# Kernel optimization log

Hardware: AMD Instinct MI355X
Metric: run time of the kernel (lower is better)

The kernel has to match this reference:

```python
import jax, jax.numpy as jnp
import numpy as np

N_QUBITS = 4
N_LAYERS = 3
SHORT_W = 2048
LONG_W = 8192
BATCH = 2048


def _conv1d(x, w, b, pad):
    # x: [B, Cin, L], w: [Cout, Cin, K]
    y = jax.lax.conv_general_dilated(x, w, window_strides=(1,), padding=[(pad, pad)],
                                     dimension_numbers=("NCH", "OIH", "NCH"))
    return y + b[None, :, None]


def _ry_mat(t):
    c, s = jnp.cos(t / 2), jnp.sin(t / 2)
    return jnp.stack([jnp.stack([c, -s]), jnp.stack([s, c])]).astype(jnp.complex64)


def _rz_mat(a):
    return jnp.diag(jnp.stack([jnp.exp(-0.5j * a), jnp.exp(0.5j * a)])).astype(jnp.complex64)


def _rot_mat(phi, theta, omega):
    # PennyLane Rot(phi, theta, omega) = RZ(omega) @ RY(theta) @ RZ(phi)
    return _rz_mat(omega) @ _ry_mat(theta) @ _rz_mat(phi)


def _apply_1q(state, U, wire):
    state = jnp.tensordot(U, state, axes=((1,), (wire,)))
    return jnp.moveaxis(state, 0, wire)


def _apply_cnot(state, c, t):
    s0 = jax.lax.index_in_dim(state, 0, axis=c, keepdims=True)
    s1 = jax.lax.index_in_dim(state, 1, axis=c, keepdims=True)
    s1 = jnp.flip(s1, axis=t)
    return jnp.concatenate([s0, s1], axis=c)


def _circuit(x, w):
    # x: [4] real features, w: [3, 4, 3] StronglyEntanglingLayers weights
    state = jnp.zeros((2,) * N_QUBITS, jnp.complex64).at[(0,) * N_QUBITS].set(1.0)
    for i in range(N_QUBITS):
        state = _apply_1q(state, _ry_mat(jnp.pi * x[i]), i)
    for l in range(N_LAYERS):
        r = (l % (N_QUBITS - 1)) + 1  # default PennyLane ranges: 1,2,3
        for i in range(N_QUBITS):
            state = _apply_1q(state, _rot_mat(w[l, i, 0], w[l, i, 1], w[l, i, 2]), i)
        for i in range(N_QUBITS):
            state = _apply_cnot(state, i, (i + r) % N_QUBITS)
    probs = jnp.abs(state) ** 2
    zs = []
    for i in range(N_QUBITS):
        p = probs.sum(axis=tuple(a for a in range(N_QUBITS) if a != i))
        zs.append(p[0] - p[1])  # <PauliZ_i>
    return jnp.stack(zs)


def setup_inputs() -> dict:
    key = jax.random.key(0)
    ks = jax.random.split(key, 13)
    d = {}
    d["xs"] = jax.random.normal(ks[0], (BATCH, 1, SHORT_W), jnp.float32)
    d["xl"] = jax.random.normal(ks[1], (BATCH, 1, LONG_W), jnp.float32)
    d["cs_conv_w"] = jax.random.normal(ks[2], (8, 1, 3), jnp.float32) * 0.3
    d["cs_conv_b"] = jax.random.normal(ks[3], (8,), jnp.float32) * 0.1
    d["cs_lin_w"] = jax.random.normal(ks[4], (2, 8 * SHORT_W), jnp.float32) * (1.0 / np.sqrt(8 * SHORT_W))
    d["cs_lin_b"] = jax.random.normal(ks[5], (2,), jnp.float32) * 0.1
    d["cl_conv_w"] = jax.random.normal(ks[6], (8, 1, 5), jnp.float32) * 0.3
    d["cl_conv_b"] = jax.random.normal(ks[7], (8,), jnp.float32) * 0.1
    d["cl_lin_w"] = jax.random.normal(ks[8], (2, 8 * LONG_W // 2), jnp.float32) * (1.0 / np.sqrt(8 * LONG_W // 2))
    d["cl_lin_b"] = jax.random.normal(ks[9], (2,), jnp.float32) * 0.1
    d["rw"] = jax.random.normal(ks[10], (N_LAYERS, N_QUBITS, 3), jnp.float32)
    d["fc_w"] = jax.random.normal(ks[11], (1, N_QUBITS), jnp.float32) * 0.5
    d["fc_b"] = jax.random.normal(ks[12], (1,), jnp.float32) * 0.1
    return d


def reference(xs, xl, cs_conv_w, cs_conv_b, cs_lin_w, cs_lin_b,
              cl_conv_w, cl_conv_b, cl_lin_w, cl_lin_b, rw, fc_w, fc_b):
    B = xs.shape[0]
    # short branch: conv(k=3,p=1) -> relu -> flatten -> linear
    hs = jax.nn.relu(_conv1d(xs, cs_conv_w, cs_conv_b, 1)).reshape(B, -1)
    fs = hs @ cs_lin_w.T + cs_lin_b  # [B, 2]
    # long branch: conv(k=5,p=2) -> relu -> maxpool(2) -> flatten -> linear
    hl = jax.nn.relu(_conv1d(xl, cl_conv_w, cl_conv_b, 2))
    hl = hl.reshape(B, 8, LONG_W // 2, 2).max(axis=-1).reshape(B, -1)
    fl = hl @ cl_lin_w.T + cl_lin_b  # [B, 2]
    f = jnp.concatenate([fs, fl], axis=1)  # [B, 4]
    # original detaches features before the quantum circuit
    f = jax.lax.stop_gradient(f)
    rw_c = jax.lax.stop_gradient(rw)
    qo = jax.vmap(lambda x: _circuit(x, rw_c))(f).astype(jnp.float32)  # [B, 4]
    return qo @ fc_w.T + fc_b  # [B, 1]
```

## Files before the change

### kernel.cpp

```cpp
#include <hip/hip_runtime.h>
#include <math.h>

namespace {
constexpr int kB  = 2048;
constexpr int kSW = 2048;
constexpr int kLW = 8192;
constexpr int kLP = kLW / 2;
constexpr int kROWS = 4;
constexpr int kNBLK = 3072;
}

__device__ __forceinline__ void long_quarter(
    int blk, int q, const float* __restrict__ xl, const float* __restrict__ cw,
    const float* __restrict__ cb, const float* __restrict__ lw,
    float* __restrict__ partL) {
  const int lane = threadIdx.x;
  const int b0 = blk * kROWS;

  float wgt[8][5], bias[8];
#pragma unroll
  for (int c = 0; c < 8; ++c) {
#pragma unroll
    for (int k = 0; k < 5; ++k) wgt[c][k] = cw[c * 5 + k];
    bias[c] = cb[c];
  }

  float acc[kROWS][2];
#pragma unroll
  for (int r = 0; r < kROWS; ++r) { acc[r][0] = 0.f; acc[r][1] = 0.f; }

  for (int ch = 0; ch < 4; ++ch) {
    const int p0 = q * 1024 + ch * 256 + lane * 4;
    const int s  = 2 * p0;

    float w[kROWS][12];
#pragma unroll
    for (int r = 0; r < kROWS; ++r) {
      const float* x = xl + (size_t)(b0 + r) * kLW;
      float2 hm = (p0 > 0) ? *reinterpret_cast<const float2*>(x + s - 2)
                           : make_float2(0.f, 0.f);
      float4 f0 = *reinterpret_cast<const float4*>(x + s);
      float4 f1 = *reinterpret_cast<const float4*>(x + s + 4);
      float2 f2 = (s + 8 < kLW) ? *reinterpret_cast<const float2*>(x + s + 8)
                                : make_float2(0.f, 0.f);
      w[r][0] = hm.x; w[r][1] = hm.y;
      w[r][2] = f0.x; w[r][3] = f0.y; w[r][4] = f0.z; w[r][5] = f0.w;
      w[r][6] = f1.x; w[r][7] = f1.y; w[r][8] = f1.z; w[r][9] = f1.w;
      w[r][10] = f2.x; w[r][11] = f2.y;
    }
    float4 la4[8], lb4[8];
#pragma unroll
    for (int c = 0; c < 8; ++c) {
      la4[c] = *reinterpret_cast<const float4*>(lw + (size_t)c * kLP + p0);
      lb4[c] = *reinterpret_cast<const float4*>(lw + (size_t)(8 + c) * kLP + p0);
    }

#pragma unroll
    for (int c = 0; c < 8; ++c) {
      const float la[4] = {la4[c].x, la4[c].y, la4[c].z, la4[c].w};
      const float lbv[4] = {lb4[c].x, lb4[c].y, lb4[c].z, lb4[c].w};
#pragma unroll
      for (int r = 0; r < kROWS; ++r) {
#pragma unroll
        for (int u = 0; u < 4; ++u) {
          float v0 = fmaf(wgt[c][0], w[r][2 * u + 0],
                     fmaf(wgt[c][1], w[r][2 * u + 1],
                     fmaf(wgt[c][2], w[r][2 * u + 2],
                     fmaf(wgt[c][3], w[r][2 * u + 3],
                     fmaf(wgt[c][4], w[r][2 * u + 4], bias[c])))));
          float v1 = fmaf(wgt[c][0], w[r][2 * u + 1],
                     fmaf(wgt[c][1], w[r][2 * u + 2],
                     fmaf(wgt[c][2], w[r][2 * u + 3],
                     fmaf(wgt[c][3], w[r][2 * u + 4],
                     fmaf(wgt[c][4], w[r][2 * u + 5], bias[c])))));
          const float m = fmaxf(fmaxf(v0, v1), 0.f);
          acc[r][0] = fmaf(m, la[u], acc[r][0]);
          acc[r][1] = fmaf(m, lbv[u], acc[r][1]);
        }
      }
    }
  }

#pragma unroll
  for (int r = 0; r < kROWS; ++r)
#pragma unroll
    for (int o = 0; o < 2; ++o) {
#pragma unroll
      for (int off = 32; off > 0; off >>= 1)
        acc[r][o] += __shfl_down(acc[r][o], off);
    }
  if (lane == 0) {
#pragma unroll
    for (int r = 0; r < kROWS; ++r) {
      partL[(size_t)q * kB * 2 + (size_t)(b0 + r) * 2 + 0] = acc[r][0];
      partL[(size_t)q * kB * 2 + (size_t)(b0 + r) * 2 + 1] = acc[r][1];
    }
  }
}

__device__ __forceinline__ void short_half(
    int blk, int h, const float* __restrict__ xs, const float* __restrict__ cw,
    const float* __restrict__ cb, const float* __restrict__ lw,
    float* __restrict__ partS) {
  const int lane = threadIdx.x;
  const int b0 = blk * kROWS;

  float wgt[8][3], bias[8];
#pragma unroll
  for (int c = 0; c < 8; ++c) {
#pragma unroll
    for (int k = 0; k < 3; ++k) wgt[c][k] = cw[c * 3 + k];
    bias[c] = cb[c];
  }

  float acc[kROWS][2];
#pragma unroll
  for (int r = 0; r < kROWS; ++r) { acc[r][0] = 0.f; acc[r][1] = 0.f; }

  for (int ch = 0; ch < 4; ++ch) {
    const int p0 = h * 1024 + ch * 256 + lane * 4;

    float w[kROWS][6];
#pragma unroll
    for (int r = 0; r < kROWS; ++r) {
      const float* x = xs + (size_t)(b0 + r) * kSW;
      float xm = (p0 > 0) ? x[p0 - 1] : 0.f;
      float4 f0 = *reinterpret_cast<const float4*>(x + p0);
      float xp = (p0 + 4 < kSW) ? x[p0 + 4] : 0.f;
      w[r][0] = xm;
      w[r][1] = f0.x; w[r][2] = f0.y; w[r][3] = f0.z; w[r][4] = f0.w;
      w[r][5] = xp;
    }
    float4 la4[8], lb4[8];
#pragma unroll
    for (int c = 0; c < 8; ++c) {
      la4[c] = *reinterpret_cast<const float4*>(lw + (size_t)c * kSW + p0);
      lb4[c] = *reinterpret_cast<const float4*>(lw + (size_t)(8 + c) * kSW + p0);
    }

#pragma unroll
    for (int c = 0; c < 8; ++c) {
      const float la[4] = {la4[c].x, la4[c].y, la4[c].z, la4[c].w};
      const float lbv[4] = {lb4[c].x, lb4[c].y, lb4[c].z, lb4[c].w};
#pragma unroll
      for (int r = 0; r < kROWS; ++r) {
#pragma unroll
        for (int u = 0; u < 4; ++u) {
          float v = fmaf(wgt[c][0], w[r][u],
                    fmaf(wgt[c][1], w[r][u + 1],
                    fmaf(wgt[c][2], w[r][u + 2], bias[c])));
          const float m = fmaxf(v, 0.f);
          acc[r][0] = fmaf(m, la[u], acc[r][0]);
          acc[r][1] = fmaf(m, lbv[u], acc[r][1]);
        }
      }
    }
  }

#pragma unroll
  for (int r = 0; r < kROWS; ++r)
#pragma unroll
    for (int o = 0; o < 2; ++o) {
#pragma unroll
      for (int off = 32; off > 0; off >>= 1)
        acc[r][o] += __shfl_down(acc[r][o], off);
    }
  if (lane == 0) {
#pragma unroll
    for (int r = 0; r < kROWS; ++r) {
      partS[(size_t)h * kB * 2 + (size_t)(b0 + r) * 2 + 0] = acc[r][0];
      partS[(size_t)h * kB * 2 + (size_t)(b0 + r) * 2 + 1] = acc[r][1];
    }
  }
}

__global__ __launch_bounds__(64, 4) void features_kernel(
    const float* __restrict__ xs, const float* __restrict__ cs_cw,
    const float* __restrict__ cs_cb, const float* __restrict__ cs_lw,
    const float* __restrict__ xl, const float* __restrict__ cl_cw,
    const float* __restrict__ cl_cb, const float* __restrict__ cl_lw,
    float* __restrict__ partS, float* __restrict__ partL) {
  const int bid = blockIdx.x;
  const int tri = bid / 3, rem = bid % 3;
  if (rem < 2) {
    const int li = tri * 2 + rem;
    long_quarter(li >> 2, li & 3, xl, cl_cw, cl_cb, cl_lw, partL);
  } else {
    const int si = tri;
    short_half(si >> 1, si & 1, xs, cs_cw, cs_cb, cs_lw, partS);
  }
}

template <int MASK>
__device__ __forceinline__ void apply_1q(float (&ar)[16], float (&ai)[16],
                                         float u00r, float u00i, float u01r, float u01i,
                                         float u10r, float u10i, float u11r, float u11i) {
#pragma unroll
  for (int i = 0; i < 16; ++i) {
    if (!(i & MASK)) {
      const int j = i | MASK;
      const float a0r = ar[i], a0i = ai[i];
      const float a1r = ar[j], a1i = ai[j];
      ar[i] = u00r * a0r - u00i * a0i + u01r * a1r - u01i * a1i;
      ai[i] = u00r * a0i + u00i * a0r + u01r * a1i + u01i * a1r;
      ar[j] = u10r * a0r - u10i * a0i + u11r * a1r - u11i * a1i;
      ai[j] = u10r * a0i + u10i * a0r + u11r * a1i + u11i * a1r;
    }
  }
}

template <int MASK>
__device__ __forceinline__ void apply_ry(float (&ar)[16], float (&ai)[16], float half_t) {
  float s, c;
  sincosf(half_t, &s, &c);
  apply_1q<MASK>(ar, ai, c, 0.f, -s, 0.f, s, 0.f, c, 0.f);
}

template <int MASK>
__device__ __forceinline__ void apply_rot(float (&ar)[16], float (&ai)[16],
                                          float phi, float theta, float omega) {
  float st, ct; sincosf(0.5f * theta, &st, &ct);
  float sa, ca; sincosf(0.5f * (phi + omega), &sa, &ca);
  float sm, cm; sincosf(0.5f * (phi - omega), &sm, &cm);
  apply_1q<MASK>(ar, ai,
                 ct * ca, -ct * sa,
                 -st * cm, -st * sm,
                 st * cm, -st * sm,
                 ct * ca, ct * sa);
}

template <int MC, int MT>
__device__ __forceinline__ void apply_cnot(float (&ar)[16], float (&ai)[16]) {
#pragma unroll
  for (int i = 0; i < 16; ++i) {
    if ((i & MC) && !(i & MT)) {
      const int j = i | MT;
      float t;
      t = ar[i]; ar[i] = ar[j]; ar[j] = t;
      t = ai[i]; ai[i] = ai[j]; ai[j] = t;
    }
  }
}

__global__ __launch_bounds__(64) void quantum_kernel(
    const float* __restrict__ partS, const float* __restrict__ partL,
    const float* __restrict__ cs_lb, const float* __restrict__ cl_lb,
    const float* __restrict__ rw, const float* __restrict__ fcw,
    const float* __restrict__ fcb, float* __restrict__ out) {
  const int b = blockIdx.x * 64 + threadIdx.x;
  if (b >= kB) return;

  const float f0 = partS[(size_t)b * 2 + 0] + partS[(size_t)kB * 2 + b * 2 + 0] + cs_lb[0];
  const float f1 = partS[(size_t)b * 2 + 1] + partS[(size_t)kB * 2 + b * 2 + 1] + cs_lb[1];
  float f2 = cl_lb[0], f3 = cl_lb[1];
#pragma unroll
  for (int q = 0; q < 4; ++q) {
    f2 += partL[(size_t)q * kB * 2 + b * 2 + 0];
    f3 += partL[(size_t)q * kB * 2 + b * 2 + 1];
  }

  float ar[16], ai[16];
#pragma unroll
  for (int i = 0; i < 16; ++i) { ar[i] = 0.f; ai[i] = 0.f; }
  ar[0] = 1.f;

  const float kHalfPi = 1.57079632679489662f;
  apply_ry<8>(ar, ai, kHalfPi * f0);
  apply_ry<4>(ar, ai, kHalfPi * f1);
  apply_ry<2>(ar, ai, kHalfPi * f2);
  apply_ry<1>(ar, ai, kHalfPi * f3);

  apply_rot<8>(ar, ai, rw[0], rw[1], rw[2]);
  apply_rot<4>(ar, ai, rw[3], rw[4], rw[5]);
  apply_rot<2>(ar, ai, rw[6], rw[7], rw[8]);
  apply_rot<1>(ar, ai, rw[9], rw[10], rw[11]);
  apply_cnot<8, 4>(ar, ai);
  apply_cnot<4, 2>(ar, ai);
  apply_cnot<2, 1>(ar, ai);
  apply_cnot<1, 8>(ar, ai);

  apply_rot<8>(ar, ai, rw[12], rw[13], rw[14]);
  apply_rot<4>(ar, ai, rw[15], rw[16], rw[17]);
  apply_rot<2>(ar, ai, rw[18], rw[19], rw[20]);
  apply_rot<1>(ar, ai, rw[21], rw[22], rw[23]);
  apply_cnot<8, 2>(ar, ai);
  apply_cnot<4, 1>(ar, ai);
  apply_cnot<2, 8>(ar, ai);
  apply_cnot<1, 4>(ar, ai);

  apply_rot<8>(ar, ai, rw[24], rw[25], rw[26]);
  apply_rot<4>(ar, ai, rw[27], rw[28], rw[29]);
  apply_rot<2>(ar, ai, rw[30], rw[31], rw[32]);
  apply_rot<1>(ar, ai, rw[33], rw[34], rw[35]);
  apply_cnot<8, 1>(ar, ai);
  apply_cnot<4, 8>(ar, ai);
  apply_cnot<2, 4>(ar, ai);
  apply_cnot<1, 2>(ar, ai);

  float z0 = 0.f, z1 = 0.f, z2 = 0.f, z3 = 0.f;
#pragma unroll
  for (int i = 0; i < 16; ++i) {
    const float p = ar[i] * ar[i] + ai[i] * ai[i];
    z0 += (i & 8) ? -p : p;
    z1 += (i & 4) ? -p : p;
    z2 += (i & 2) ? -p : p;
    z3 += (i & 1) ? -p : p;
  }
  out[b] = fcb[0] + z0 * fcw[0] + z1 * fcw[1] + z2 * fcw[2] + z3 * fcw[3];
}

extern "C" void kernel_launch(void* const* d_in, const int* in_sizes, int n_in,
                              void* d_out, int out_size, void* d_ws, size_t ws_size,
                              hipStream_t stream) {
  const float* xs     = (const float*)d_in[0];
  const float* xl     = (const float*)d_in[1];
  const float* cs_cw  = (const float*)d_in[2];
  const float* cs_cb  = (const float*)d_in[3];
  const float* cs_lw  = (const float*)d_in[4];
  const float* cs_lb  = (const float*)d_in[5];
  const float* cl_cw  = (const float*)d_in[6];
  const float* cl_cb  = (const float*)d_in[7];
  const float* cl_lw  = (const float*)d_in[8];
  const float* cl_lb  = (const float*)d_in[9];
  const float* rw     = (const float*)d_in[10];
  const float* fcw    = (const float*)d_in[11];
  const float* fcb    = (const float*)d_in[12];
  float* out   = (float*)d_out;
  float* partS = (float*)d_ws;
  float* partL = (float*)d_ws + 2 * kB * 2;

  hipLaunchKernelGGL(features_kernel, dim3(kNBLK), dim3(64), 0, stream,
                     xs, cs_cw, cs_cb, cs_lw,
                     xl, cl_cw, cl_cb, cl_lw, partS, partL);
  hipLaunchKernelGGL(quantum_kernel, dim3(kB / 64), dim3(64), 0, stream,
                     partS, partL, cs_lb, cl_lb, rw, fcw, fcb, out);
}
```

Baseline: 52.11 us.

## Keep linear weights in registers and loop over 16 rows per wave

Reworks the feature kernel so each wave owns a narrow column slice (128 pooled positions for long, 256 for short) and iterates over 16 batch rows. The slice of the linear weights is loaded into registers once and reused across all rows, where before it was reloaded per chunk for every group of 4 rows. This cuts repeated weight traffic. In exchange there are more partial slices (32 long, 8 short), a larger workspace, more per-row shuffle reductions and more partial sums for the quantum kernel to read.

```diff
diff --git a/kernel.cpp b/kernel.cpp
--- a/kernel.cpp
+++ b/kernel.cpp
@@ -6,16 +6,18 @@
 constexpr int kSW = 2048;
 constexpr int kLW = 8192;
 constexpr int kLP = kLW / 2;
-constexpr int kROWS = 4;
-constexpr int kNBLK = 3072;
-}
-
-__device__ __forceinline__ void long_quarter(
-    int blk, int q, const float* __restrict__ xl, const float* __restrict__ cw,
+constexpr int kR  = 16;
+constexpr int kNBLK = 5120;
+}
+
+__device__ __forceinline__ void long_slice(
+    int grp, int sl, const float* __restrict__ xl, const float* __restrict__ cw,
     const float* __restrict__ cb, const float* __restrict__ lw,
     float* __restrict__ partL) {
   const int lane = threadIdx.x;
-  const int b0 = blk * kROWS;
+  const int b0 = grp * kR;
+  const int p0 = sl * 128 + lane * 2;
+  const int s  = 2 * p0;
 
   float wgt[8][5], bias[8];
 #pragma unroll
@@ -25,85 +27,68 @@
     bias[c] = cb[c];
   }
 
-  float acc[kROWS][2];
-#pragma unroll
-  for (int r = 0; r < kROWS; ++r) { acc[r][0] = 0.f; acc[r][1] = 0.f; }
-
-  for (int ch = 0; ch < 4; ++ch) {
-    const int p0 = q * 1024 + ch * 256 + lane * 4;
-    const int s  = 2 * p0;
-
-    float w[kROWS][12];
-#pragma unroll
-    for (int r = 0; r < kROWS; ++r) {
-      const float* x = xl + (size_t)(b0 + r) * kLW;
-      float2 hm = (p0 > 0) ? *reinterpret_cast<const float2*>(x + s - 2)
-                           : make_float2(0.f, 0.f);
-      float4 f0 = *reinterpret_cast<const float4*>(x + s);
-      float4 f1 = *reinterpret_cast<const float4*>(x + s + 4);
-      float2 f2 = (s + 8 < kLW) ? *reinterpret_cast<const float2*>(x + s + 8)
-                                : make_float2(0.f, 0.f);
-      w[r][0] = hm.x; w[r][1] = hm.y;
-      w[r][2] = f0.x; w[r][3] = f0.y; w[r][4] = f0.z; w[r][5] = f0.w;
-      w[r][6] = f1.x; w[r][7] = f1.y; w[r][8] = f1.z; w[r][9] = f1.w;
-      w[r][10] = f2.x; w[r][11] = f2.y;
-    }
-    float4 la4[8], lb4[8];
+  float la[8][2], lb[8][2];
+#pragma unroll
+  for (int c = 0; c < 8; ++c) {
+    float2 a2 = *reinterpret_cast<const float2*>(lw + (size_t)c * kLP + p0);
+    float2 b2 = *reinterpret_cast<const float2*>(lw + (size_t)(8 + c) * kLP + p0);
+    la[c][0] = a2.x; la[c][1] = a2.y;
+    lb[c][0] = b2.x; lb[c][1] = b2.y;
+  }
+
+  const bool lo_ok = (p0 > 0);
+  const bool hi_ok = (s + 4 < kLW);
+
+  for (int r = 0; r < kR; ++r) {
+    const float* x = xl + (size_t)(b0 + r) * kLW;
+    float2 hm = lo_ok ? *reinterpret_cast<const float2*>(x + s - 2)
+                      : make_float2(0.f, 0.f);
+    float4 f0 = *reinterpret_cast<const float4*>(x + s);
+    float2 f1 = hi_ok ? *reinterpret_cast<const float2*>(x + s + 4)
+                      : make_float2(0.f, 0.f);
+    float W[8];
+    W[0] = hm.x; W[1] = hm.y;
+    W[2] = f0.x; W[3] = f0.y; W[4] = f0.z; W[5] = f0.w;
+    W[6] = f1.x; W[7] = f1.y;
+
+    float a0 = 0.f, a1 = 0.f;
 #pragma unroll
     for (int c = 0; c < 8; ++c) {
-      la4[c] = *reinterpret_cast<const float4*>(lw + (size_t)c * kLP + p0);
-      lb4[c] = *reinterpret_cast<const float4*>(lw + (size_t)(8 + c) * kLP + p0);
-    }
-
-#pragma unroll
-    for (int c = 0; c < 8; ++c) {
-      const float la[4] = {la4[c].x, la4[c].y, la4[c].z, la4[c].w};
-      const float lbv[4] = {lb4[c].x, lb4[c].y, lb4[c].z, lb4[c].w};
-#pragma unroll
-      for (int r = 0; r < kROWS; ++r) {
-#pragma unroll
-        for (int u = 0; u < 4; ++u) {
-          float v0 = fmaf(wgt[c][0], w[r][2 * u + 0],
-                     fmaf(wgt[c][1], w[r][2 * u + 1],
-                     fmaf(wgt[c][2], w[r][2 * u + 2],
-                     fmaf(wgt[c][3], w[r][2 * u + 3],
-                     fmaf(wgt[c][4], w[r][2 * u + 4], bias[c])))));
-          float v1 = fmaf(wgt[c][0], w[r][2 * u + 1],
-                     fmaf(wgt[c][1], w[r][2 * u + 2],
-                     fmaf(wgt[c][2], w[r][2 * u + 3],
-                     fmaf(wgt[c][3], w[r][2 * u + 4],
-                     fmaf(wgt[c][4], w[r][2 * u + 5], bias[c])))));
-          const float m = fmaxf(fmaxf(v0, v1), 0.f);
-          acc[r][0] = fmaf(m, la[u], acc[r][0]);
-          acc[r][1] = fmaf(m, lbv[u], acc[r][1]);
-        }
+#pragma unroll
+      for (int u = 0; u < 2; ++u) {
+        float v0 = fmaf(wgt[c][0], W[2 * u + 0],
+                   fmaf(wgt[c][1], W[2 * u + 1],
+                   fmaf(wgt[c][2], W[2 * u + 2],
+                   fmaf(wgt[c][3], W[2 * u + 3],
+                   fmaf(wgt[c][4], W[2 * u + 4], bias[c])))));
+        float v1 = fmaf(wgt[c][0], W[2 * u + 1],
+                   fmaf(wgt[c][1], W[2 * u + 2],
+                   fmaf(wgt[c][2], W[2 * u + 3],
+                   fmaf(wgt[c][3], W[2 * u + 4],
+                   fmaf(wgt[c][4], W[2 * u + 5], bias[c])))));
+        const float m = fmaxf(fmaxf(v0, v1), 0.f);
+        a0 = fmaf(m, la[c][u], a0);
+        a1 = fmaf(m, lb[c][u], a1);
       }
     }
-  }
-
-#pragma unroll
-  for (int r = 0; r < kROWS; ++r)
-#pragma unroll
-    for (int o = 0; o < 2; ++o) {
-#pragma unroll
-      for (int off = 32; off > 0; off >>= 1)
-        acc[r][o] += __shfl_down(acc[r][o], off);
-    }
-  if (lane == 0) {
-#pragma unroll
-    for (int r = 0; r < kROWS; ++r) {
-      partL[(size_t)q * kB * 2 + (size_t)(b0 + r) * 2 + 0] = acc[r][0];
-      partL[(size_t)q * kB * 2 + (size_t)(b0 + r) * 2 + 1] = acc[r][1];
-    }
-  }
-}
-
-__device__ __forceinline__ void short_half(
-    int blk, int h, const float* __restrict__ xs, const float* __restrict__ cw,
+#pragma unroll
+    for (int off = 32; off > 0; off >>= 1) {
+      a0 += __shfl_down(a0, off);
+      a1 += __shfl_down(a1, off);
+    }
+    if (lane == 0)
+      *reinterpret_cast<float2*>(partL + (size_t)sl * kB * 2 + (size_t)(b0 + r) * 2) =
+          make_float2(a0, a1);
+  }
+}
+
+__device__ __forceinline__ void short_slice(
+    int grp, int sl, const float* __restrict__ xs, const float* __restrict__ cw,
     const float* __restrict__ cb, const float* __restrict__ lw,
     float* __restrict__ partS) {
   const int lane = threadIdx.x;
-  const int b0 = blk * kROWS;
+  const int b0 = grp * kR;
+  const int p0 = sl * 256 + lane * 4;
 
   float wgt[8][3], bias[8];
 #pragma unroll
@@ -113,64 +98,49 @@
     bias[c] = cb[c];
   }
 
-  float acc[kROWS][2];
-#pragma unroll
-  for (int r = 0; r < kROWS; ++r) { acc[r][0] = 0.f; acc[r][1] = 0.f; }
-
-  for (int ch = 0; ch < 4; ++ch) {
-    const int p0 = h * 1024 + ch * 256 + lane * 4;
-
-    float w[kROWS][6];
-#pragma unroll
-    for (int r = 0; r < kROWS; ++r) {
-      const float* x = xs + (size_t)(b0 + r) * kSW;
-      float xm = (p0 > 0) ? x[p0 - 1] : 0.f;
-      float4 f0 = *reinterpret_cast<const float4*>(x + p0);
-      float xp = (p0 + 4 < kSW) ? x[p0 + 4] : 0.f;
-      w[r][0] = xm;
-      w[r][1] = f0.x; w[r][2] = f0.y; w[r][3] = f0.z; w[r][4] = f0.w;
-      w[r][5] = xp;
-    }
-    float4 la4[8], lb4[8];
+  float la[8][4], lb[8][4];
+#pragma unroll
+  for (int c = 0; c < 8; ++c) {
+    float4 a4 = *reinterpret_cast<const float4*>(lw + (size_t)c * kSW + p0);
+    float4 b4 = *reinterpret_cast<const float4*>(lw + (size_t)(8 + c) * kSW + p0);
+    la[c][0] = a4.x; la[c][1] = a4.y; la[c][2] = a4.z; la[c][3] = a4.w;
+    lb[c][0] = b4.x; lb[c][1] = b4.y; lb[c][2] = b4.z; lb[c][3] = b4.w;
+  }
+
+  const bool lo_ok = (p0 > 0);
+  const bool hi_ok = (p0 + 4 < kSW);
+
+  for (int r = 0; r < kR; ++r) {
+    const float* x = xs + (size_t)(b0 + r) * kSW;
+    float xm = lo_ok ? x[p0 - 1] : 0.f;
+    float4 f0 = *reinterpret_cast<const float4*>(x + p0);
+    float xp = hi_ok ? x[p0 + 4] : 0.f;
+    float W[6];
+    W[0] = xm;
+    W[1] = f0.x; W[2] = f0.y; W[3] = f0.z; W[4] = f0.w;
+    W[5] = xp;
+
+    float a0 = 0.f, a1 = 0.f;
 #pragma unroll
     for (int c = 0; c < 8; ++c) {
-      la4[c] = *reinterpret_cast<const float4*>(lw + (size_t)c * kSW + p0);
-      lb4[c] = *reinterpret_cast<const float4*>(lw + (size_t)(8 + c) * kSW + p0);
-    }
-
-#pragma unroll
-    for (int c = 0; c < 8; ++c) {
-      const float la[4] = {la4[c].x, la4[c].y, la4[c].z, la4[c].w};
-      const float lbv[4] = {lb4[c].x, lb4[c].y, lb4[c].z, lb4[c].w};
-#pragma unroll
-      for (int r = 0; r < kROWS; ++r) {
-#pragma unroll
-        for (int u = 0; u < 4; ++u) {
-          float v = fmaf(wgt[c][0], w[r][u],
-                    fmaf(wgt[c][1], w[r][u + 1],
-                    fmaf(wgt[c][2], w[r][u + 2], bias[c])));
-          const float m = fmaxf(v, 0.f);
-          acc[r][0] = fmaf(m, la[u], acc[r][0]);
-          acc[r][1] = fmaf(m, lbv[u], acc[r][1]);
-        }
+#pragma unroll
+      for (int u = 0; u < 4; ++u) {
+        float v = fmaf(wgt[c][0], W[u],
+                  fmaf(wgt[c][1], W[u + 1],
+                  fmaf(wgt[c][2], W[u + 2], bias[c])));
+        const float m = fmaxf(v, 0.f);
+        a0 = fmaf(m, la[c][u], a0);
+        a1 = fmaf(m, lb[c][u], a1);
       }
     }
-  }
-
-#pragma unroll
-  for (int r = 0; r < kROWS; ++r)
-#pragma unroll
-    for (int o = 0; o < 2; ++o) {
-#pragma unroll
-      for (int off = 32; off > 0; off >>= 1)
-        acc[r][o] += __shfl_down(acc[r][o], off);
-    }
-  if (lane == 0) {
-#pragma unroll
-    for (int r = 0; r < kROWS; ++r) {
-      partS[(size_t)h * kB * 2 + (size_t)(b0 + r) * 2 + 0] = acc[r][0];
-      partS[(size_t)h * kB * 2 + (size_t)(b0 + r) * 2 + 1] = acc[r][1];
-    }
+#pragma unroll
+    for (int off = 32; off > 0; off >>= 1) {
+      a0 += __shfl_down(a0, off);
+      a1 += __shfl_down(a1, off);
+    }
+    if (lane == 0)
+      *reinterpret_cast<float2*>(partS + (size_t)sl * kB * 2 + (size_t)(b0 + r) * 2) =
+          make_float2(a0, a1);
   }
 }
 
@@ -181,13 +151,13 @@
     const float* __restrict__ cl_cb, const float* __restrict__ cl_lw,
     float* __restrict__ partS, float* __restrict__ partL) {
   const int bid = blockIdx.x;
-  const int tri = bid / 3, rem = bid % 3;
-  if (rem < 2) {
-    const int li = tri * 2 + rem;
-    long_quarter(li >> 2, li & 3, xl, cl_cw, cl_cb, cl_lw, partL);
+  const int grp5 = bid / 5, rem = bid % 5;
+  if (rem < 4) {
+    const int li = grp5 * 4 + rem;
+    long_slice(li >> 5, li & 31, xl, cl_cw, cl_cb, cl_lw, partL);
   } else {
-    const int si = tri;
-    short_half(si >> 1, si & 1, xs, cs_cw, cs_cb, cs_lw, partS);
+    const int si = grp5;
+    short_slice(si >> 3, si & 7, xs, cs_cw, cs_cb, cs_lw, partS);
   }
 }
 
@@ -250,13 +220,17 @@
   const int b = blockIdx.x * 64 + threadIdx.x;
   if (b >= kB) return;
 
-  const float f0 = partS[(size_t)b * 2 + 0] + partS[(size_t)kB * 2 + b * 2 + 0] + cs_lb[0];
-  const float f1 = partS[(size_t)b * 2 + 1] + partS[(size_t)kB * 2 + b * 2 + 1] + cs_lb[1];
+  float f0 = cs_lb[0], f1 = cs_lb[1];
+#pragma unroll
+  for (int sl = 0; sl < 8; ++sl) {
+    float2 p = *reinterpret_cast<const float2*>(partS + (size_t)sl * kB * 2 + b * 2);
+    f0 += p.x; f1 += p.y;
+  }
   float f2 = cl_lb[0], f3 = cl_lb[1];
 #pragma unroll
-  for (int q = 0; q < 4; ++q) {
-    f2 += partL[(size_t)q * kB * 2 + b * 2 + 0];
-    f3 += partL[(size_t)q * kB * 2 + b * 2 + 1];
+  for (int sl = 0; sl < 32; ++sl) {
+    float2 p = *reinterpret_cast<const float2*>(partL + (size_t)sl * kB * 2 + b * 2);
+    f2 += p.x; f3 += p.y;
   }
 
   float ar[16], ai[16];
@@ -327,7 +301,7 @@
   const float* fcb    = (const float*)d_in[12];
   float* out   = (float*)d_out;
   float* partS = (float*)d_ws;
-  float* partL = (float*)d_ws + 2 * kB * 2;
+  float* partL = (float*)d_ws + 8 * kB * 2;
 
   hipLaunchKernelGGL(features_kernel, dim3(kNBLK), dim3(64), 0, stream,
                      xs, cs_cw, cs_cb, cs_lw,
```

After: 55.64 us. 6.8% more time.

## Retile feature kernel to 256-thread blocks with per-thread position and multi-row reuse

Applied to the files above, without the earlier changes.

Restructures the conv/linear feature kernel so each 256-thread block handles one slice of positions across 16 (long) or 8 (short) batch rows. Each thread holds its linear weights in registers and reuses them across all rows. Wave partials are combined through shared memory into more slices, and the quantum kernel sums those slices. The intent is less redundant weight traffic and better occupancy. The cost is narrower float2 input loads with overlapping halos and a larger shuffle reduction.

```diff
diff --git a/kernel.cpp b/kernel.cpp
--- a/kernel.cpp
+++ b/kernel.cpp
@@ -6,16 +6,22 @@
 constexpr int kSW = 2048;
 constexpr int kLW = 8192;
 constexpr int kLP = kLW / 2;
-constexpr int kROWS = 4;
-constexpr int kNBLK = 3072;
-}
-
-__device__ __forceinline__ void long_quarter(
-    int blk, int q, const float* __restrict__ xl, const float* __restrict__ cw,
+constexpr int kLR = 16;
+constexpr int kSR = 8;
+constexpr int kLSL = 16;
+constexpr int kSSL = 4;
+constexpr int kLBLK = kLSL * (kB / kLR);
+constexpr int kSBLK = kSSL * (kB / kSR);
+constexpr int kNBLK = kLBLK + kSBLK;
+}
+
+__device__ __forceinline__ void long_path(
+    int sl, int rg, const float* __restrict__ xl, const float* __restrict__ cw,
     const float* __restrict__ cb, const float* __restrict__ lw,
-    float* __restrict__ partL) {
-  const int lane = threadIdx.x;
-  const int b0 = blk * kROWS;
+    float* __restrict__ partL, float (*red)[32]) {
+  const int t = threadIdx.x;
+  const int b0 = rg * kLR;
+  const int P = sl * 256 + t;
 
   float wgt[8][5], bias[8];
 #pragma unroll
@@ -25,85 +31,77 @@
     bias[c] = cb[c];
   }
 
-  float acc[kROWS][2];
-#pragma unroll
-  for (int r = 0; r < kROWS; ++r) { acc[r][0] = 0.f; acc[r][1] = 0.f; }
-
-  for (int ch = 0; ch < 4; ++ch) {
-    const int p0 = q * 1024 + ch * 256 + lane * 4;
-    const int s  = 2 * p0;
-
-    float w[kROWS][12];
-#pragma unroll
-    for (int r = 0; r < kROWS; ++r) {
-      const float* x = xl + (size_t)(b0 + r) * kLW;
-      float2 hm = (p0 > 0) ? *reinterpret_cast<const float2*>(x + s - 2)
-                           : make_float2(0.f, 0.f);
-      float4 f0 = *reinterpret_cast<const float4*>(x + s);
-      float4 f1 = *reinterpret_cast<const float4*>(x + s + 4);
-      float2 f2 = (s + 8 < kLW) ? *reinterpret_cast<const float2*>(x + s + 8)
-                                : make_float2(0.f, 0.f);
-      w[r][0] = hm.x; w[r][1] = hm.y;
-      w[r][2] = f0.x; w[r][3] = f0.y; w[r][4] = f0.z; w[r][5] = f0.w;
-      w[r][6] = f1.x; w[r][7] = f1.y; w[r][8] = f1.z; w[r][9] = f1.w;
-      w[r][10] = f2.x; w[r][11] = f2.y;
-    }
-    float4 la4[8], lb4[8];
+  float la[8], lb[8];
+#pragma unroll
+  for (int c = 0; c < 8; ++c) {
+    la[c] = lw[(size_t)c * kLP + P];
+    lb[c] = lw[(size_t)(8 + c) * kLP + P];
+  }
+
+  float acc0[kLR], acc1[kLR];
+#pragma unroll
+  for (int r = 0; r < kLR; ++r) { acc0[r] = 0.f; acc1[r] = 0.f; }
+
+  const bool lo = (P > 0);
+  const bool hi = (P < kLP - 1);
+  const float* xb = xl + (size_t)b0 * kLW + 2 * P;
+
+#pragma unroll
+  for (int r = 0; r < kLR; ++r) {
+    const float* x = xb + (size_t)r * kLW;
+    float2 A = lo ? *reinterpret_cast<const float2*>(x - 2) : make_float2(0.f, 0.f);
+    float2 Bv = *reinterpret_cast<const float2*>(x);
+    float2 C = hi ? *reinterpret_cast<const float2*>(x + 2) : make_float2(0.f, 0.f);
+    const float W0 = A.x, W1 = A.y, W2 = Bv.x, W3 = Bv.y, W4 = C.x, W5 = C.y;
 #pragma unroll
     for (int c = 0; c < 8; ++c) {
-      la4[c] = *reinterpret_cast<const float4*>(lw + (size_t)c * kLP + p0);
-      lb4[c] = *reinterpret_cast<const float4*>(lw + (size_t)(8 + c) * kLP + p0);
-    }
-
-#pragma unroll
-    for (int c = 0; c < 8; ++c) {
-      const float la[4] = {la4[c].x, la4[c].y, la4[c].z, la4[c].w};
-      const float lbv[4] = {lb4[c].x, lb4[c].y, lb4[c].z, lb4[c].w};
-#pragma unroll
-      for (int r = 0; r < kROWS; ++r) {
-#pragma unroll
-        for (int u = 0; u < 4; ++u) {
-          float v0 = fmaf(wgt[c][0], w[r][2 * u + 0],
-                     fmaf(wgt[c][1], w[r][2 * u + 1],
-                     fmaf(wgt[c][2], w[r][2 * u + 2],
-                     fmaf(wgt[c][3], w[r][2 * u + 3],
-                     fmaf(wgt[c][4], w[r][2 * u + 4], bias[c])))));
-          float v1 = fmaf(wgt[c][0], w[r][2 * u + 1],
-                     fmaf(wgt[c][1], w[r][2 * u + 2],
-                     fmaf(wgt[c][2], w[r][2 * u + 3],
-                     fmaf(wgt[c][3], w[r][2 * u + 4],
-                     fmaf(wgt[c][4], w[r][2 * u + 5], bias[c])))));
-          const float m = fmaxf(fmaxf(v0, v1), 0.f);
-          acc[r][0] = fmaf(m, la[u], acc[r][0]);
-          acc[r][1] = fmaf(m, lbv[u], acc[r][1]);
-        }
-      }
-    }
-  }
-
-#pragma unroll
-  for (int r = 0; r < kROWS; ++r)
-#pragma unroll
-    for (int o = 0; o < 2; ++o) {
-#pragma unroll
-      for (int off = 32; off > 0; off >>= 1)
-        acc[r][o] += __shfl_down(acc[r][o], off);
-    }
+      float v0 = fmaf(wgt[c][0], W0,
+                 fmaf(wgt[c][1], W1,
+                 fmaf(wgt[c][2], W2,
+                 fmaf(wgt[c][3], W3,
+                 fmaf(wgt[c][4], W4, bias[c])))));
+      float v1 = fmaf(wgt[c][0], W1,
+                 fmaf(wgt[c][1], W2,
+                 fmaf(wgt[c][2], W3,
+                 fmaf(wgt[c][3], W4,
+                 fmaf(wgt[c][4], W5, bias[c])))));
+      const float m = fmaxf(fmaxf(v0, v1), 0.f);
+      acc0[r] = fmaf(m, la[c], acc0[r]);
+      acc1[r] = fmaf(m, lb[c], acc1[r]);
+    }
+  }
+
+#pragma unroll
+  for (int m = 1; m < 64; m <<= 1) {
+#pragma unroll
+    for (int r = 0; r < kLR; ++r) {
+      acc0[r] += __shfl_xor(acc0[r], m);
+      acc1[r] += __shfl_xor(acc1[r], m);
+    }
+  }
+  const int w = t >> 6, lane = t & 63;
   if (lane == 0) {
 #pragma unroll
-    for (int r = 0; r < kROWS; ++r) {
-      partL[(size_t)q * kB * 2 + (size_t)(b0 + r) * 2 + 0] = acc[r][0];
-      partL[(size_t)q * kB * 2 + (size_t)(b0 + r) * 2 + 1] = acc[r][1];
-    }
-  }
-}
-
-__device__ __forceinline__ void short_half(
-    int blk, int h, const float* __restrict__ xs, const float* __restrict__ cw,
+    for (int r = 0; r < kLR; ++r) {
+      red[w][r] = acc0[r];
+      red[w][kLR + r] = acc1[r];
+    }
+  }
+  __syncthreads();
+  if (t < 2 * kLR) {
+    const int o = t >> 4, r = t & 15;
+    const float s = red[0][t] + red[1][t] + red[2][t] + red[3][t];
+    partL[(size_t)sl * kB * 2 + (size_t)(b0 + r) * 2 + o] = s;
+  }
+}
+
+__device__ __forceinline__ void short_path(
+    int sl, int rg, const float* __restrict__ xs, const float* __restrict__ cw,
     const float* __restrict__ cb, const float* __restrict__ lw,
-    float* __restrict__ partS) {
-  const int lane = threadIdx.x;
-  const int b0 = blk * kROWS;
+    float* __restrict__ partS, float (*red)[32]) {
+  const int t = threadIdx.x;
+  const int b0 = rg * kSR;
+  const int q = sl * 512 + 2 * t;
 
   float wgt[8][3], bias[8];
 #pragma unroll
@@ -113,81 +111,84 @@
     bias[c] = cb[c];
   }
 
-  float acc[kROWS][2];
-#pragma unroll
-  for (int r = 0; r < kROWS; ++r) { acc[r][0] = 0.f; acc[r][1] = 0.f; }
-
-  for (int ch = 0; ch < 4; ++ch) {
-    const int p0 = h * 1024 + ch * 256 + lane * 4;
-
-    float w[kROWS][6];
-#pragma unroll
-    for (int r = 0; r < kROWS; ++r) {
-      const float* x = xs + (size_t)(b0 + r) * kSW;
-      float xm = (p0 > 0) ? x[p0 - 1] : 0.f;
-      float4 f0 = *reinterpret_cast<const float4*>(x + p0);
-      float xp = (p0 + 4 < kSW) ? x[p0 + 4] : 0.f;
-      w[r][0] = xm;
-      w[r][1] = f0.x; w[r][2] = f0.y; w[r][3] = f0.z; w[r][4] = f0.w;
-      w[r][5] = xp;
-    }
-    float4 la4[8], lb4[8];
+  float la0[8], la1[8], lb0[8], lb1[8];
+#pragma unroll
+  for (int c = 0; c < 8; ++c) {
+    float2 a = *reinterpret_cast<const float2*>(lw + (size_t)c * kSW + q);
+    float2 b = *reinterpret_cast<const float2*>(lw + (size_t)(8 + c) * kSW + q);
+    la0[c] = a.x; la1[c] = a.y;
+    lb0[c] = b.x; lb1[c] = b.y;
+  }
+
+  float acc0[kSR], acc1[kSR];
+#pragma unroll
+  for (int r = 0; r < kSR; ++r) { acc0[r] = 0.f; acc1[r] = 0.f; }
+
+  const bool lo = (q > 0);
+  const bool hi = (q < kSW - 2);
+  const float* xb = xs + (size_t)b0 * kSW + q;
+
+#pragma unroll
+  for (int r = 0; r < kSR; ++r) {
+    const float* x = xb + (size_t)r * kSW;
+    float2 A = lo ? *reinterpret_cast<const float2*>(x - 2) : make_float2(0.f, 0.f);
+    float2 Bv = *reinterpret_cast<const float2*>(x);
+    float2 C = hi ? *reinterpret_cast<const float2*>(x + 2) : make_float2(0.f, 0.f);
+    const float W1 = A.y, W2 = Bv.x, W3 = Bv.y, W4 = C.x;
 #pragma unroll
     for (int c = 0; c < 8; ++c) {
-      la4[c] = *reinterpret_cast<const float4*>(lw + (size_t)c * kSW + p0);
-      lb4[c] = *reinterpret_cast<const float4*>(lw + (size_t)(8 + c) * kSW + p0);
-    }
-
-#pragma unroll
-    for (int c = 0; c < 8; ++c) {
-      const float la[4] = {la4[c].x, la4[c].y, la4[c].z, la4[c].w};
-      const float lbv[4] = {lb4[c].x, lb4[c].y, lb4[c].z, lb4[c].w};
-#pragma unroll
-      for (int r = 0; r < kROWS; ++r) {
-#pragma unroll
-        for (int u = 0; u < 4; ++u) {
-          float v = fmaf(wgt[c][0], w[r][u],
-                    fmaf(wgt[c][1], w[r][u + 1],
-                    fmaf(wgt[c][2], w[r][u + 2], bias[c])));
-          const float m = fmaxf(v, 0.f);
-          acc[r][0] = fmaf(m, la[u], acc[r][0]);
-          acc[r][1] = fmaf(m, lbv[u], acc[r][1]);
-        }
-      }
-    }
-  }
-
-#pragma unroll
-  for (int r = 0; r < kROWS; ++r)
-#pragma unroll
-    for (int o = 0; o < 2; ++o) {
-#pragma unroll
-      for (int off = 32; off > 0; off >>= 1)
-        acc[r][o] += __shfl_down(acc[r][o], off);
-    }
+      float v0 = fmaf(wgt[c][0], W1,
+                 fmaf(wgt[c][1], W2,
+                 fmaf(wgt[c][2], W3, bias[c])));
+      float v1 = fmaf(wgt[c][0], W2,
+                 fmaf(wgt[c][1], W3,
+                 fmaf(wgt[c][2], W4, bias[c])));
+      const float m0 = fmaxf(v0, 0.f);
+      const float m1 = fmaxf(v1, 0.f);
+      acc0[r] = fmaf(m1, la1[c], fmaf(m0, la0[c], acc0[r]));
+      acc1[r] = fmaf(m1, lb1[c], fmaf(m0, lb0[c], acc1[r]));
+    }
+  }
+
+#pragma unroll
+  for (int m = 1; m < 64; m <<= 1) {
+#pragma unroll
+    for (int r = 0; r < kSR; ++r) {
+      acc0[r] += __shfl_xor(acc0[r], m);
+      acc1[r] += __shfl_xor(acc1[r], m);
+    }
+  }
+  const int w = t >> 6, lane = t & 63;
   if (lane == 0) {
 #pragma unroll
-    for (int r = 0; r < kROWS; ++r) {
-      partS[(size_t)h * kB * 2 + (size_t)(b0 + r) * 2 + 0] = acc[r][0];
-      partS[(size_t)h * kB * 2 + (size_t)(b0 + r) * 2 + 1] = acc[r][1];
-    }
-  }
-}
-
-__global__ __launch_bounds__(64, 4) void features_kernel(
+    for (int r = 0; r < kSR; ++r) {
+      red[w][r] = acc0[r];
+      red[w][kSR + r] = acc1[r];
+    }
+  }
+  __syncthreads();
+  if (t < 2 * kSR) {
+    const int o = t >> 3, r = t & 7;
+    const float s = red[0][t] + red[1][t] + red[2][t] + red[3][t];
+    partS[(size_t)sl * kB * 2 + (size_t)(b0 + r) * 2 + o] = s;
+  }
+}
+
+__global__ __launch_bounds__(256, 4) void features_kernel(
     const float* __restrict__ xs, const float* __restrict__ cs_cw,
     const float* __restrict__ cs_cb, const float* __restrict__ cs_lw,
     const float* __restrict__ xl, const float* __restrict__ cl_cw,
     const float* __restrict__ cl_cb, const float* __restrict__ cl_lw,
     float* __restrict__ partS, float* __restrict__ partL) {
+  __shared__ float red[4][32];
   const int bid = blockIdx.x;
   const int tri = bid / 3, rem = bid % 3;
   if (rem < 2) {
     const int li = tri * 2 + rem;
-    long_quarter(li >> 2, li & 3, xl, cl_cw, cl_cb, cl_lw, partL);
+    long_path(li >> 7, li & 127, xl, cl_cw, cl_cb, cl_lw, partL, red);
   } else {
     const int si = tri;
-    short_half(si >> 1, si & 1, xs, cs_cw, cs_cb, cs_lw, partS);
+    short_path(si >> 8, si & 255, xs, cs_cw, cs_cb, cs_lw, partS, red);
   }
 }
 
@@ -250,13 +251,17 @@
   const int b = blockIdx.x * 64 + threadIdx.x;
   if (b >= kB) return;
 
-  const float f0 = partS[(size_t)b * 2 + 0] + partS[(size_t)kB * 2 + b * 2 + 0] + cs_lb[0];
-  const float f1 = partS[(size_t)b * 2 + 1] + partS[(size_t)kB * 2 + b * 2 + 1] + cs_lb[1];
+  float f0 = cs_lb[0], f1 = cs_lb[1];
+#pragma unroll
+  for (int sl = 0; sl < kSSL; ++sl) {
+    float2 p = *reinterpret_cast<const float2*>(partS + (size_t)sl * kB * 2 + b * 2);
+    f0 += p.x; f1 += p.y;
+  }
   float f2 = cl_lb[0], f3 = cl_lb[1];
 #pragma unroll
-  for (int q = 0; q < 4; ++q) {
-    f2 += partL[(size_t)q * kB * 2 + b * 2 + 0];
-    f3 += partL[(size_t)q * kB * 2 + b * 2 + 1];
+  for (int sl = 0; sl < kLSL; ++sl) {
+    float2 p = *reinterpret_cast<const float2*>(partL + (size_t)sl * kB * 2 + b * 2);
+    f2 += p.x; f3 += p.y;
   }
 
   float ar[16], ai[16];
@@ -327,9 +332,9 @@
   const float* fcb    = (const float*)d_in[12];
   float* out   = (float*)d_out;
   float* partS = (float*)d_ws;
-  float* partL = (float*)d_ws + 2 * kB * 2;
-
-  hipLaunchKernelGGL(features_kernel, dim3(kNBLK), dim3(64), 0, stream,
+  float* partL = (float*)d_ws + kSSL * kB * 2;
+
+  hipLaunchKernelGGL(features_kernel, dim3(kNBLK), dim3(256), 0, stream,
                      xs, cs_cw, cs_cb, cs_lw,
                      xl, cl_cw, cl_cb, cl_lw, partS, partL);
   hipLaunchKernelGGL(quantum_kernel, dim3(kB / 64), dim3(64), 0, stream,
```

After: 53.38 us. +2.4%, slower.
